# Performance work log

Hardware: AMD Instinct MI355X
Metric: run time of the kernel (lower is better)

Reference implementation:

```python
import jax, jax.numpy as jnp
import numpy as np

RMIN, RMAX, MAX_PHASE = 0.9, 1.0, 6.283


def setup_inputs() -> dict:
    key = jax.random.key(0)
    ks = jax.random.split(key, 12)
    Bsz, T, U, O, S, H = 16, 4096, 128, 128, 256, 512
    inp = jax.random.normal(ks[0], (Bsz, T, U), dtype=jnp.float32)
    # stable complex diagonal: |lambda| in [RMIN, RMAX], phase in [0, MAX_PHASE]
    r = RMIN + (RMAX - RMIN) * jax.random.uniform(ks[1], (S,), dtype=jnp.float32)
    theta = MAX_PHASE * jax.random.uniform(ks[2], (S,), dtype=jnp.float32)
    Lambda_re = r * jnp.cos(theta)
    Lambda_im = r * jnp.sin(theta)
    B = jax.random.normal(ks[3], (S, U), dtype=jnp.float32) / np.sqrt(U)
    C = jax.random.normal(ks[4], (O, S), dtype=jnp.float32) / np.sqrt(S)
    D = jax.random.normal(ks[5], (O, U), dtype=jnp.float32) / np.sqrt(U)
    W1 = jax.random.normal(ks[6], (H, O), dtype=jnp.float32) / np.sqrt(O)
    W2 = jax.random.normal(ks[7], (H, H), dtype=jnp.float32) / np.sqrt(H)
    W3 = jax.random.normal(ks[8], (O, H), dtype=jnp.float32) / np.sqrt(H)
    Wlin = jax.random.normal(ks[9], (O, U), dtype=jnp.float32) / np.sqrt(U)
    return {"input": inp, "Lambda_re": Lambda_re, "Lambda_im": Lambda_im,
            "B": B, "C": C, "D": D, "W1": W1, "W2": W2, "W3": W3, "Wlin": Wlin}


def _linear_scan(lam, bu):
    # lam: (S,) complex; bu: (B, T, S) complex
    # h_t = lam * h_{t-1} + bu_t, h_0 = 0  (work-efficient associative scan)
    A = jnp.broadcast_to(lam[None, None, :], bu.shape)

    def combine(c1, c2):
        a1, x1 = c1
        a2, x2 = c2
        return a1 * a2, a2 * x1 + x2

    _, h = jax.lax.associative_scan(combine, (A, bu), axis=1)
    return h


def reference(input, Lambda_re, Lambda_im, B, C, D, W1, W2, W3, Wlin):
    lam = (Lambda_re + 1j * Lambda_im).astype(jnp.complex64)        # (S,)
    bu = jnp.einsum('btu,su->bts', input, B).astype(jnp.complex64)   # (B,T,S)
    h = _linear_scan(lam, bu)                                        # (B,T,S) complex
    # LRU readout: real(C h) + D u
    y = jnp.einsum('bts,os->bto', h, C.astype(jnp.complex64)).real \
        + jnp.einsum('btu,ou->bto', input, D)                        # (B,T,O)
    # MLP: Linear->SiLU->Linear->ReLU->Linear (no biases)
    z = jax.nn.silu(y @ W1.T)
    z = jax.nn.relu(z @ W2.T)
    mlp_out = z @ W3.T                                               # (B,T,O)
    # residual linear path
    return mlp_out + input @ Wlin.T
```

## Files before the change

### kernel.cpp

```cpp
#include <hip/hip_runtime.h>
#include <hip/hip_bf16.h>

#define BSZ 16
#define TT 4096
#define UU 128
#define OO 128
#define SS 256
#define HH 512
#define BT (BSZ*TT)
#define CLEN 64
#define NCH (TT/CLEN)

using bf16x8 = __attribute__((ext_vector_type(8))) short;
using f32x4  = __attribute__((ext_vector_type(4))) float;

__device__ __forceinline__ unsigned short f2bf(float x){
  union { float f; unsigned int u; } v; v.f = x;
  unsigned int r = v.u + 0x7fffu + ((v.u >> 16) & 1u);
  return (unsigned short)(r >> 16);
}
__device__ __forceinline__ float bf2f(unsigned short h){
  union { float f; unsigned int u; } v; v.u = ((unsigned int)h) << 16;
  return v.f;
}

#define GLD16(g, s) __builtin_amdgcn_global_load_lds( \
    (const __attribute__((address_space(1))) unsigned int*)(g), \
    (__attribute__((address_space(3))) unsigned int*)(s), 16, 0, 0)

#define SBAR() do{ __builtin_amdgcn_sched_barrier(0); \
                   __builtin_amdgcn_s_barrier(); \
                   __builtin_amdgcn_sched_barrier(0); }while(0)

__global__ __launch_bounds__(256) void split_k(const float* __restrict__ x,
                                               unsigned short* __restrict__ H,
                                               unsigned short* __restrict__ L, int n4){
  int i = blockIdx.x * 256 + threadIdx.x;
  if (i >= n4) return;
  float4 v = ((const float4*)x)[i];
  unsigned short h0 = f2bf(v.x), h1 = f2bf(v.y), h2 = f2bf(v.z), h3 = f2bf(v.w);
  ushort4 hh = make_ushort4(h0, h1, h2, h3);
  ushort4 ll = make_ushort4(f2bf(v.x - bf2f(h0)), f2bf(v.y - bf2f(h1)),
                            f2bf(v.z - bf2f(h2)), f2bf(v.w - bf2f(h3)));
  ((ushort4*)H)[i] = hh;
  ((ushort4*)L)[i] = ll;
}

struct WJobs {
  const float* src[7];
  unsigned short* H[7];
  unsigned short* L[7];
  int end4[7];
};
__global__ __launch_bounds__(256) void split_w(WJobs j, int total4){
  int i = blockIdx.x * 256 + threadIdx.x;
  if (i >= total4) return;
  int t = 0, base = 0;
  #pragma unroll
  for (int k = 0; k < 7; k++){
    if (i >= j.end4[k]){ t = k + 1; base = j.end4[k]; }
  }
  int idx = i - base;
  float4 v = ((const float4*)j.src[t])[idx];
  unsigned short h0 = f2bf(v.x), h1 = f2bf(v.y), h2 = f2bf(v.z), h3 = f2bf(v.w);
  ushort4 hh = make_ushort4(h0, h1, h2, h3);
  ushort4 ll = make_ushort4(f2bf(v.x - bf2f(h0)), f2bf(v.y - bf2f(h1)),
                            f2bf(v.z - bf2f(h2)), f2bf(v.w - bf2f(h3)));
  ((ushort4*)j.H[t])[idx] = hh;
  ((ushort4*)j.L[t])[idx] = ll;
}

__global__ __launch_bounds__(256, 2) void gemm_split(
    const unsigned short* __restrict__ AH1, const unsigned short* __restrict__ AL1,
    const unsigned short* __restrict__ BH1, const unsigned short* __restrict__ BL1, int K1, int f1,
    const unsigned short* __restrict__ AH2, const unsigned short* __restrict__ AL2,
    const unsigned short* __restrict__ BH2, const unsigned short* __restrict__ BL2, int K2, int f2,
    unsigned short* __restrict__ outH, unsigned short* __restrict__ outL,
    float* __restrict__ outF, int Nout, int EPI,
    const float* __restrict__ lre, const float* __restrict__ lim,
    float2* __restrict__ ends)
{
  __shared__ __align__(16) unsigned short SM[32768];
  unsigned short* Ah = SM;
  unsigned short* Al = SM + 8192;
  unsigned short* Bh = SM + 16384;
  unsigned short* Bl = SM + 24576;

  const int tid = threadIdx.x;
  const int mb = blockIdx.x, nb = blockIdx.y;
  const int l = tid & 63, w = tid >> 6;
  const int wr = w >> 1, wc = w & 1;
  const int fr = l & 15, fq = l >> 4;

  f32x4 acc[4][4];
  #pragma unroll
  for (int m = 0; m < 4; m++)
    #pragma unroll
    for (int n = 0; n < 4; n++) acc[m][n] = f32x4{0.f, 0.f, 0.f, 0.f};

  const int nkt = (K1 + K2) >> 5;

  auto STAGE = [&](int buf, int kt){
    const int k0 = kt << 5;
    const unsigned short *aH, *aL, *bH, *bL; int st, kk, flg;
    if (k0 < K1){ aH = AH1; aL = AL1; bH = BH1; bL = BL1; st = K1; kk = k0; flg = f1; }
    else        { aH = AH2; aL = AL2; bH = BH2; bL = BL2; st = K2; kk = k0 - K1; flg = f2; }
    #pragma unroll
    for (int it = 0; it < 2; it++){
      int seg = tid + it * 256;
      int r = seg >> 2, c4 = seg & 3;
      int sc = (c4 ^ ((r >> 1) & 3)) << 3;
      size_t go = (size_t)(mb*128 + r) * st + kk + sc;
      size_t gb = (size_t)(nb*128 + r) * st + kk + sc;
      int lo = buf*4096 + r*32 + c4*8;
      GLD16(aH + go, Ah + lo);
      if (flg & 1) GLD16(aL + go, Al + lo);
      GLD16(bH + gb, Bh + lo);
      if (flg & 2) GLD16(bL + gb, Bl + lo);
    }
  };

  STAGE(0, 0);
  __syncthreads();

  for (int kt = 0; kt < nkt; kt++){
    const int cur = kt & 1;
    const int flg = ((kt << 5) < K1) ? f1 : f2;
    if (kt + 1 < nkt) STAGE(cur ^ 1, kt + 1);

    bf16x8 a_h[4], a_l[4], b_h[4], b_l[4];
    #pragma unroll
    for (int m = 0; m < 4; m++){
      int lra = wr*64 + m*16 + fr;
      int ra = cur*4096 + lra*32 + ((fq ^ ((lra >> 1) & 3)) << 3);
      a_h[m] = *(const bf16x8*)&Ah[ra];
      if (flg & 1) a_l[m] = *(const bf16x8*)&Al[ra];
      int lrb = wc*64 + m*16 + fr;
      int rb = cur*4096 + lrb*32 + ((fq ^ ((lrb >> 1) & 3)) << 3);
      b_h[m] = *(const bf16x8*)&Bh[rb];
      if (flg & 2) b_l[m] = *(const bf16x8*)&Bl[rb];
    }
    __builtin_amdgcn_s_setprio(1);
    #pragma unroll
    for (int m = 0; m < 4; m++)
      #pragma unroll
      for (int n = 0; n < 4; n++)
        acc[m][n] = __builtin_amdgcn_mfma_f32_16x16x32_bf16(a_h[m], b_h[n], acc[m][n], 0, 0, 0);
    if (flg & 1)
      #pragma unroll
      for (int m = 0; m < 4; m++)
        #pragma unroll
        for (int n = 0; n < 4; n++)
          acc[m][n] = __builtin_amdgcn_mfma_f32_16x16x32_bf16(a_l[m], b_h[n], acc[m][n], 0, 0, 0);
    if (flg & 2)
      #pragma unroll
      for (int m = 0; m < 4; m++)
        #pragma unroll
        for (int n = 0; n < 4; n++)
          acc[m][n] = __builtin_amdgcn_mfma_f32_16x16x32_bf16(a_h[m], b_l[n], acc[m][n], 0, 0, 0);
    __builtin_amdgcn_s_setprio(0);

    __syncthreads();
  }

  float* fl = (float*)SM;
  #pragma unroll
  for (int m = 0; m < 4; m++)
    #pragma unroll
    for (int n = 0; n < 4; n++)
      #pragma unroll
      for (int j = 0; j < 4; j++)
        fl[(wr*64 + m*16 + fq*4 + j)*128 + wc*64 + n*16 + fr] = acc[m][n][j];
  __syncthreads();
  #pragma unroll
  for (int it = 0; it < 8; it++){
    int task = tid + (it << 8);
    int rl = task >> 4, cg = task & 15;
    float4 v0 = *(const float4*)&fl[rl*128 + cg*8];
    float4 v1 = *(const float4*)&fl[rl*128 + cg*8 + 4];
    size_t o = (size_t)(mb*128 + rl) * Nout + nb*128 + cg*8;
    if (EPI == 0){
      *(float4*)(outF + o)     = v0;
      *(float4*)(outF + o + 4) = v1;
    } else {
      float xv[8] = {v0.x,v0.y,v0.z,v0.w,v1.x,v1.y,v1.z,v1.w};
      union { unsigned short us[8]; uint4 v; } ph, pl;
      #pragma unroll
      for (int e = 0; e < 8; e++){
        float x = xv[e];
        if (EPI == 2)      x = x / (1.f + __expf(-x));
        else if (EPI == 3) x = fmaxf(x, 0.f);
        ph.us[e] = f2bf(x);
        pl.us[e] = f2bf(x - bf2f(ph.us[e]));
      }
      *(uint4*)(outH + o) = ph.v;
      if (outL) *(uint4*)(outL + o) = pl.v;
    }
  }
  if (ends){
    int c = tid >> 7, sl = tid & 127;
    int b = mb >> 5, chunk = ((mb & 31) << 1) + c;
    int s = nb*128 + sl;
    float lr = lre[s], li = lim[s];
    float hr = 0.f, hi2 = 0.f;
    for (int t = 0; t < 64; t++){
      float x = fl[(c*64 + t)*128 + sl];
      float nr = fmaf(lr, hr, fmaf(-li, hi2, x));
      float ni = fmaf(lr, hi2, li * hr);
      hr = nr; hi2 = ni;
    }
    ends[((size_t)(b*NCH + chunk))*SS + s] = make_float2(hr, hi2);
  }
}

#define WS_OFF 65536
#define YOFF   131072

__global__ __launch_bounds__(512, 1) void mlp_fused(
    const unsigned short* __restrict__ yH,
    const unsigned short* __restrict__ W1H,
    const unsigned short* __restrict__ W2H,
    unsigned short* __restrict__ z2H)
{
  __shared__ __align__(16) unsigned char LDS[163840];
  const int tid = threadIdx.x;
  const int l = tid & 63, w = tid >> 6;
  const int fr = l & 15, fq = l >> 4;
  const size_t r0 = (size_t)blockIdx.x * 64;

  const unsigned short* w2base[4];
  int w2lds[4];
  #pragma unroll
  for (int it = 0; it < 4; it++){
    int seg = l + (it << 6);
    int r = seg >> 2, c4 = seg & 3;
    w2base[it] = W2H + (size_t)(w*64 + r) * HH + ((c4 ^ ((r >> 1) & 3)) << 3);
    w2lds[it] = WS_OFF + w*12288 + seg*16;
  }
  auto stageW2 = [&](int kt){
    const int so = (kt % 3) * 4096;
    #pragma unroll
    for (int it = 0; it < 4; it++)
      GLD16(w2base[it] + kt*32, LDS + w2lds[it] + so);
  };

  #pragma unroll
  for (int it = 0; it < 16; it++){
    int seg = tid + (it << 9);
    int r = seg >> 4, c16 = seg & 15;
    GLD16(W1H + (size_t)r * UU + ((c16 ^ (r & 7)) << 3), LDS + seg*16);
  }
  #pragma unroll
  for (int it = 0; it < 2; it++){
    int seg = tid + (it << 9);
    int r = seg >> 4, c16 = seg & 15;
    GLD16(yH + (size_t)(r0 + r) * UU + ((c16 ^ (r & 7)) << 3),
          LDS + YOFF + seg*16);
  }
  asm volatile("s_waitcnt vmcnt(0)" ::: "memory");
  SBAR();

  f32x4 acc[4][4];
  #pragma unroll
  for (int m = 0; m < 4; m++)
    #pragma unroll
    for (int n = 0; n < 4; n++) acc[m][n] = f32x4{0.f, 0.f, 0.f, 0.f};

  #pragma unroll
  for (int kt = 0; kt < 4; kt++){
    bf16x8 a[4], b[4];
    #pragma unroll
    for (int m = 0; m < 4; m++){
      int row = m*16 + fr, kc = kt*4 + fq;
      a[m] = *(const bf16x8*)(LDS + YOFF + (row*128 + ((kc ^ (row & 7)) << 3))*2);
    }
    #pragma unroll
    for (int n = 0; n < 4; n++){
      int lrb = w*64 + n*16 + fr, kc = kt*4 + fq;
      b[n] = *(const bf16x8*)(LDS + (lrb*128 + ((kc ^ (lrb & 7)) << 3))*2);
    }
    __builtin_amdgcn_s_setprio(1);
    #pragma unroll
    for (int m = 0; m < 4; m++)
      #pragma unroll
      for (int n = 0; n < 4; n++)
        acc[m][n] = __builtin_amdgcn_mfma_f32_16x16x32_bf16(a[m], b[n], acc[m][n], 0, 0, 0);
    __builtin_amdgcn_s_setprio(0);
  }
  SBAR();

  stageW2(0);
  stageW2(1);

  unsigned short* Z1 = (unsigned short*)LDS;
  #pragma unroll
  for (int m = 0; m < 4; m++)
    #pragma unroll
    for (int n = 0; n < 4; n++)
      #pragma unroll
      for (int j = 0; j < 4; j++){
        float x = acc[m][n][j];
        x = x / (1.f + __expf(-x));
        int row = m*16 + fq*4 + j;
        int col = w*64 + n*16 + fr;
        Z1[(col >> 3)*512 + row*8 + (col & 7)] = f2bf(x);
      }
  SBAR();

  #pragma unroll
  for (int m = 0; m < 4; m++)
    #pragma unroll
    for (int n = 0; n < 4; n++) acc[m][n] = f32x4{0.f, 0.f, 0.f, 0.f};

  for (int kt = 0; kt < 16; kt++){
    if (kt < 15) asm volatile("s_waitcnt vmcnt(4)" ::: "memory");
    else         asm volatile("s_waitcnt vmcnt(0)" ::: "memory");
    __builtin_amdgcn_sched_barrier(0);
    const unsigned char* Wb = LDS + WS_OFF + w*12288 + (kt % 3)*4096;
    bf16x8 a[4], b[4];
    #pragma unroll
    for (int m = 0; m < 4; m++)
      a[m] = *(const bf16x8*)(LDS + (size_t)(kt*4 + fq)*1024 + (m*16 + fr)*16);
    #pragma unroll
    for (int n = 0; n < 4; n++){
      int rl = n*16 + fr;
      b[n] = *(const bf16x8*)(Wb + rl*64 + ((fq ^ ((rl >> 1) & 3)) << 4));
    }
    __builtin_amdgcn_s_setprio(1);
    #pragma unroll
    for (int m = 0; m < 4; m++)
      #pragma unroll
      for (int n = 0; n < 4; n++)
        acc[m][n] = __builtin_amdgcn_mfma_f32_16x16x32_bf16(a[m], b[n], acc[m][n], 0, 0, 0);
    __builtin_amdgcn_s_setprio(0);
    if (kt + 2 < 16) stageW2(kt + 2);
  }
  SBAR();

  unsigned short* EP = (unsigned short*)(LDS + WS_OFF);
  #pragma unroll
  for (int m = 0; m < 4; m++)
    #pragma unroll
    for (int n = 0; n < 4; n++)
      #pragma unroll
      for (int j = 0; j < 4; j++){
        float x = fmaxf(acc[m][n][j], 0.f);
        EP[(m*16 + fq*4 + j)*512 + w*64 + n*16 + fr] = f2bf(x);
      }
  __syncthreads();
  #pragma unroll
  for (int it = 0; it < 8; it++){
    int seg = tid + (it << 9);
    int r = seg >> 6, c8 = seg & 63;
    *(uint4*)(z2H + (r0 + r)*HH + c8*8) = *(const uint4*)&EP[r*512 + c8*8];
  }
}

__global__ __launch_bounds__(256) void scan_carries(const float2* __restrict__ ends,
                                                    const float* __restrict__ lre,
                                                    const float* __restrict__ lim,
                                                    float2* __restrict__ carryin){
  const int idx = blockIdx.x * 256 + threadIdx.x;
  const int b = idx >> 8;
  const int s = idx & 255;
  float pr = lre[s], pi = lim[s];
  #pragma unroll
  for (int q = 0; q < 6; q++){
    float nr = pr*pr - pi*pi;
    float ni = 2.f * pr * pi;
    pr = nr; pi = ni;
  }
  float hr = 0.f, hi = 0.f;
  for (int c = 0; c < NCH; c++){
    size_t o = ((size_t)b*NCH + c)*SS + s;
    carryin[o] = make_float2(hr, hi);
    float2 e = ends[o];
    float nr = fmaf(pr, hr, fmaf(-pi, hi, e.x));
    float ni = fmaf(pr, hi, fmaf(pi, hr, e.y));
    hr = nr; hi = ni;
  }
}

__global__ __launch_bounds__(256) void scan_apply_v(
    const unsigned short* __restrict__ buH, const unsigned short* __restrict__ buL,
    const float* __restrict__ lre, const float* __restrict__ lim,
    const float2* __restrict__ carryin, unsigned short* __restrict__ RehH){
  const int tid = threadIdx.x;
  const int grp = tid >> 6, ln = tid & 63;
  const int chunk = blockIdx.x * 4 + grp;
  const int b = chunk >> 6, ch = chunk & 63;
  const int s0 = ln * 4;
  float lr[4], li[4], hr[4], hi[4];
  #pragma unroll
  for (int e = 0; e < 4; e++){ lr[e] = lre[s0+e]; li[e] = lim[s0+e]; }
  const float2* ci = &carryin[((size_t)(b*NCH + ch))*SS + s0];
  #pragma unroll
  for (int e = 0; e < 4; e++){ hr[e] = ci[e].x; hi[e] = ci[e].y; }
  const size_t rbase = ((size_t)b*TT + (size_t)ch*CLEN)*SS + s0;
  for (int t = 0; t < CLEN; t++){
    uint2 hv = *(const uint2*)(buH + rbase + (size_t)t*SS);
    uint2 lv = *(const uint2*)(buL + rbase + (size_t)t*SS);
    const unsigned short* hs = (const unsigned short*)&hv;
    const unsigned short* ls = (const unsigned short*)&lv;
    uint2 ov; unsigned short* os = (unsigned short*)&ov;
    #pragma unroll
    for (int e = 0; e < 4; e++){
      float x = bf2f(hs[e]) + bf2f(ls[e]);
      float nr = fmaf(lr[e], hr[e], fmaf(-li[e], hi[e], x));
      float ni = fmaf(lr[e], hi[e], li[e] * hr[e]);
      hr[e] = nr; hi[e] = ni;
      os[e] = f2bf(nr);
    }
    *(uint2*)(RehH + rbase + (size_t)t*SS) = ov;
  }
}

extern "C" void kernel_launch(void* const* d_in, const int* in_sizes, int n_in,
                              void* d_out, int out_size, void* d_ws, size_t ws_size,
                              hipStream_t stream){
  const float* inp = (const float*)d_in[0];
  const float* lre = (const float*)d_in[1];
  const float* lim = (const float*)d_in[2];
  const float* Bm  = (const float*)d_in[3];
  const float* Cm  = (const float*)d_in[4];
  const float* Dm  = (const float*)d_in[5];
  const float* W1  = (const float*)d_in[6];
  const float* W2  = (const float*)d_in[7];
  const float* W3  = (const float*)d_in[8];
  const float* Wl  = (const float*)d_in[9];
  float* out = (float*)d_out;

  char* ws = (char*)d_ws;
  size_t off = 0;
  auto alloc = [&](size_t bytes)->char*{
    char* p = ws + off; off += (bytes + 255) & ~(size_t)255; return p;
  };
  unsigned short* inH  = (unsigned short*)alloc((size_t)BT*UU*2);
  unsigned short* inL  = (unsigned short*)alloc((size_t)BT*UU*2);
  char* Rbu = alloc((size_t)BT*SS*2*2);
  unsigned short* buH = (unsigned short*)Rbu;
  unsigned short* buL = (unsigned short*)(Rbu + (size_t)BT*SS*2);
  char* R2 = alloc((size_t)BT*HH*2);
  unsigned short* RehH = (unsigned short*)R2;
  unsigned short* yH   = (unsigned short*)(R2 + (size_t)BT*SS*2);
  unsigned short* z2H  = (unsigned short*)Rbu;
  unsigned short* BwH = (unsigned short*)alloc((size_t)SS*UU*2);
  unsigned short* BwL = (unsigned short*)alloc((size_t)SS*UU*2);
  unsigned short* CH_ = (unsigned short*)alloc((size_t)OO*SS*2);
  unsigned short* CL_ = (unsigned short*)alloc((size_t)OO*SS*2);
  unsigned short* DH_ = (unsigned short*)alloc((size_t)OO*UU*2);
  unsigned short* DL_ = (unsigned short*)alloc((size_t)OO*UU*2);
  unsigned short* W1H = (unsigned short*)alloc((size_t)HH*OO*2);
  unsigned short* W1L = (unsigned short*)alloc((size_t)HH*OO*2);
  unsigned short* W2H = (unsigned short*)alloc((size_t)HH*HH*2);
  unsigned short* W2L = (unsigned short*)alloc((size_t)HH*HH*2);
  unsigned short* W3H = (unsigned short*)alloc((size_t)OO*HH*2);
  unsigned short* W3L = (unsigned short*)alloc((size_t)OO*HH*2);
  unsigned short* WlH = (unsigned short*)alloc((size_t)OO*UU*2);
  unsigned short* WlL = (unsigned short*)alloc((size_t)OO*UU*2);
  float2* ends    = (float2*)alloc((size_t)BSZ*NCH*SS*8);
  float2* carryin = (float2*)alloc((size_t)BSZ*NCH*SS*8);
  if (off > ws_size) return;

  split_k<<<(BT*UU/4 + 255)/256, 256, 0, stream>>>(inp, inH, inL, BT*UU/4);
  {
    WJobs j;
    const float* srcs[7] = {Bm, Cm, Dm, W1, W2, W3, Wl};
    unsigned short* Hs[7] = {BwH, CH_, DH_, W1H, W2H, W3H, WlH};
    unsigned short* Ls[7] = {BwL, CL_, DL_, W1L, W2L, W3L, WlL};
    int n4s[7] = {SS*UU/4, OO*SS/4, OO*UU/4, HH*OO/4, HH*HH/4, OO*HH/4, OO*UU/4};
    int cum = 0;
    for (int k = 0; k < 7; k++){
      j.src[k] = srcs[k]; j.H[k] = Hs[k]; j.L[k] = Ls[k];
      cum += n4s[k]; j.end4[k] = cum;
    }
    split_w<<<(cum + 255)/256, 256, 0, stream>>>(j, cum);
  }

  gemm_split<<<dim3(BT/128, SS/128), 256, 0, stream>>>(
      inH, inL, BwH, BwL, UU, 3,
      inH, inL, BwH, BwL, 0,  3,
      buH, buL, nullptr, SS, 1,
      lre, lim, ends);

  scan_carries<<<(BSZ*SS)/256, 256, 0, stream>>>(ends, lre, lim, carryin);

  scan_apply_v<<<BSZ*NCH/4, 256, 0, stream>>>(buH, buL, lre, lim, carryin, RehH);

  gemm_split<<<dim3(BT/128, OO/128), 256, 0, stream>>>(
      RehH, RehH, CH_, CL_, SS, 2,
      inH,  inL,  DH_, DL_, UU, 3,
      yH, nullptr, nullptr, OO, 1,
      nullptr, nullptr, nullptr);

  mlp_fused<<<BT/64, 512, 0, stream>>>(yH, W1H, W2H, z2H);

  gemm_split<<<dim3(BT/128, OO/128), 256, 0, stream>>>(
      z2H, z2H, W3H, W3L, HH, 2,
      inH, inL, WlH, WlL, UU, 3,
      nullptr, nullptr, out, OO, 0,
      nullptr, nullptr, nullptr);
}
```

Measured before the change: 207.6 us.

## Split fused MLP across 16 waves and stream W1 through the LDS ring

The fused MLP kernel now runs with 1024 threads instead of 512. Each of the 16 waves computes 32 output columns instead of 64, which halves per-wave accumulators and B fragments. W1 is no longer loaded whole into LDS up front. It is streamed in k-slices through the same triple-buffered per-wave ring as W2, so the first GEMM overlaps global loads with MFMA work and LDS use shrinks. The cost is that every wave re-reads the shared A (y / Z1) fragments, so LDS read traffic for A roughly doubles, and the block uses more barriers.

Result: no change. 204.8 us (-1.4%).

```diff
diff --git a/kernel.cpp b/kernel.cpp
--- a/kernel.cpp
+++ b/kernel.cpp
@@ -213,10 +213,9 @@
   }
 }
 
-#define WS_OFF 65536
-#define YOFF   131072
-
-__global__ __launch_bounds__(512, 1) void mlp_fused(
+#define RING_OFF 65536
+
+__global__ __launch_bounds__(1024, 1) void mlp_fused(
     const unsigned short* __restrict__ yH,
     const unsigned short* __restrict__ W1H,
     const unsigned short* __restrict__ W2H,
@@ -228,64 +227,68 @@
   const int fr = l & 15, fq = l >> 4;
   const size_t r0 = (size_t)blockIdx.x * 64;
 
-  const unsigned short* w2base[4];
-  int w2lds[4];
-  #pragma unroll
-  for (int it = 0; it < 4; it++){
+  const unsigned short* w1base[2];
+  const unsigned short* w2base[2];
+  int rlds[2];
+  #pragma unroll
+  for (int it = 0; it < 2; it++){
     int seg = l + (it << 6);
     int r = seg >> 2, c4 = seg & 3;
-    w2base[it] = W2H + (size_t)(w*64 + r) * HH + ((c4 ^ ((r >> 1) & 3)) << 3);
-    w2lds[it] = WS_OFF + w*12288 + seg*16;
-  }
+    int sc = (c4 ^ ((r >> 1) & 3)) << 3;
+    w1base[it] = W1H + (size_t)(w*32 + r) * UU + sc;
+    w2base[it] = W2H + (size_t)(w*32 + r) * HH + sc;
+    rlds[it] = RING_OFF + w*6144 + seg*16;
+  }
+  auto stageW1 = [&](int kt){
+    const int so = (kt % 3) * 2048;
+    #pragma unroll
+    for (int it = 0; it < 2; it++) GLD16(w1base[it] + kt*32, LDS + rlds[it] + so);
+  };
   auto stageW2 = [&](int kt){
-    const int so = (kt % 3) * 4096;
-    #pragma unroll
-    for (int it = 0; it < 4; it++)
-      GLD16(w2base[it] + kt*32, LDS + w2lds[it] + so);
+    const int so = (kt % 3) * 2048;
+    #pragma unroll
+    for (int it = 0; it < 2; it++) GLD16(w2base[it] + kt*32, LDS + rlds[it] + so);
   };
 
-  #pragma unroll
-  for (int it = 0; it < 16; it++){
-    int seg = tid + (it << 9);
-    int r = seg >> 4, c16 = seg & 15;
-    GLD16(W1H + (size_t)r * UU + ((c16 ^ (r & 7)) << 3), LDS + seg*16);
-  }
-  #pragma unroll
-  for (int it = 0; it < 2; it++){
-    int seg = tid + (it << 9);
-    int r = seg >> 4, c16 = seg & 15;
-    GLD16(yH + (size_t)(r0 + r) * UU + ((c16 ^ (r & 7)) << 3),
-          LDS + YOFF + seg*16);
-  }
-  asm volatile("s_waitcnt vmcnt(0)" ::: "memory");
+  {
+    int r = tid >> 4, c16 = tid & 15;
+    GLD16(yH + (size_t)(r0 + r) * UU + ((c16 ^ (r & 7)) << 3), LDS + tid*16);
+  }
+  stageW1(0);
+  stageW1(1);
+  asm volatile("s_waitcnt vmcnt(4)" ::: "memory");
   SBAR();
 
-  f32x4 acc[4][4];
+  f32x4 acc[4][2];
   #pragma unroll
   for (int m = 0; m < 4; m++)
     #pragma unroll
-    for (int n = 0; n < 4; n++) acc[m][n] = f32x4{0.f, 0.f, 0.f, 0.f};
-
-  #pragma unroll
+    for (int n = 0; n < 2; n++) acc[m][n] = f32x4{0.f, 0.f, 0.f, 0.f};
+
   for (int kt = 0; kt < 4; kt++){
-    bf16x8 a[4], b[4];
+    if (kt < 3) asm volatile("s_waitcnt vmcnt(2)" ::: "memory");
+    else        asm volatile("s_waitcnt vmcnt(0)" ::: "memory");
+    __builtin_amdgcn_sched_barrier(0);
+    const unsigned char* Wb = LDS + RING_OFF + w*6144 + (kt % 3)*2048;
+    bf16x8 a[4], b[2];
     #pragma unroll
     for (int m = 0; m < 4; m++){
       int row = m*16 + fr, kc = kt*4 + fq;
-      a[m] = *(const bf16x8*)(LDS + YOFF + (row*128 + ((kc ^ (row & 7)) << 3))*2);
-    }
-    #pragma unroll
-    for (int n = 0; n < 4; n++){
-      int lrb = w*64 + n*16 + fr, kc = kt*4 + fq;
-      b[n] = *(const bf16x8*)(LDS + (lrb*128 + ((kc ^ (lrb & 7)) << 3))*2);
+      a[m] = *(const bf16x8*)(LDS + (row*128 + ((kc ^ (row & 7)) << 3))*2);
+    }
+    #pragma unroll
+    for (int n = 0; n < 2; n++){
+      int rl = n*16 + fr;
+      b[n] = *(const bf16x8*)(Wb + rl*64 + ((fq ^ ((rl >> 1) & 3)) << 4));
     }
     __builtin_amdgcn_s_setprio(1);
     #pragma unroll
     for (int m = 0; m < 4; m++)
       #pragma unroll
-      for (int n = 0; n < 4; n++)
+      for (int n = 0; n < 2; n++)
         acc[m][n] = __builtin_amdgcn_mfma_f32_16x16x32_bf16(a[m], b[n], acc[m][n], 0, 0, 0);
     __builtin_amdgcn_s_setprio(0);
+    if (kt + 2 < 4) stageW1(kt + 2);
   }
   SBAR();
 
@@ -296,13 +299,13 @@
   #pragma unroll
   for (int m = 0; m < 4; m++)
     #pragma unroll
-    for (int n = 0; n < 4; n++)
+    for (int n = 0; n < 2; n++)
       #pragma unroll
       for (int j = 0; j < 4; j++){
         float x = acc[m][n][j];
         x = x / (1.f + __expf(-x));
         int row = m*16 + fq*4 + j;
-        int col = w*64 + n*16 + fr;
+        int col = w*32 + n*16 + fr;
         Z1[(col >> 3)*512 + row*8 + (col & 7)] = f2bf(x);
       }
   SBAR();
@@ -310,19 +313,19 @@
   #pragma unroll
   for (int m = 0; m < 4; m++)
     #pragma unroll
-    for (int n = 0; n < 4; n++) acc[m][n] = f32x4{0.f, 0.f, 0.f, 0.f};
+    for (int n = 0; n < 2; n++) acc[m][n] = f32x4{0.f, 0.f, 0.f, 0.f};
 
   for (int kt = 0; kt < 16; kt++){
-    if (kt < 15) asm volatile("s_waitcnt vmcnt(4)" ::: "memory");
+    if (kt < 15) asm volatile("s_waitcnt vmcnt(2)" ::: "memory");
     else         asm volatile("s_waitcnt vmcnt(0)" ::: "memory");
     __builtin_amdgcn_sched_barrier(0);
-    const unsigned char* Wb = LDS + WS_OFF + w*12288 + (kt % 3)*4096;
-    bf16x8 a[4], b[4];
+    const unsigned char* Wb = LDS + RING_OFF + w*6144 + (kt % 3)*2048;
+    bf16x8 a[4], b[2];
     #pragma unroll
     for (int m = 0; m < 4; m++)
       a[m] = *(const bf16x8*)(LDS + (size_t)(kt*4 + fq)*1024 + (m*16 + fr)*16);
     #pragma unroll
-    for (int n = 0; n < 4; n++){
+    for (int n = 0; n < 2; n++){
       int rl = n*16 + fr;
       b[n] = *(const bf16x8*)(Wb + rl*64 + ((fq ^ ((rl >> 1) & 3)) << 4));
     }
@@ -330,27 +333,27 @@
     #pragma unroll
     for (int m = 0; m < 4; m++)
       #pragma unroll
-      for (int n = 0; n < 4; n++)
+      for (int n = 0; n < 2; n++)
         acc[m][n] = __builtin_amdgcn_mfma_f32_16x16x32_bf16(a[m], b[n], acc[m][n], 0, 0, 0);
     __builtin_amdgcn_s_setprio(0);
     if (kt + 2 < 16) stageW2(kt + 2);
   }
   SBAR();
 
-  unsigned short* EP = (unsigned short*)(LDS + WS_OFF);
+  unsigned short* EP = (unsigned short*)(LDS + RING_OFF);
   #pragma unroll
   for (int m = 0; m < 4; m++)
     #pragma unroll
-    for (int n = 0; n < 4; n++)
+    for (int n = 0; n < 2; n++)
       #pragma unroll
       for (int j = 0; j < 4; j++){
         float x = fmaxf(acc[m][n][j], 0.f);
-        EP[(m*16 + fq*4 + j)*512 + w*64 + n*16 + fr] = f2bf(x);
+        EP[(m*16 + fq*4 + j)*512 + w*32 + n*16 + fr] = f2bf(x);
       }
   __syncthreads();
   #pragma unroll
-  for (int it = 0; it < 8; it++){
-    int seg = tid + (it << 9);
+  for (int it = 0; it < 4; it++){
+    int seg = tid + (it << 10);
     int r = seg >> 6, c8 = seg & 63;
     *(uint4*)(z2H + (r0 + r)*HH + c8*8) = *(const uint4*)&EP[r*512 + c8*8];
   }
@@ -493,7 +496,7 @@
       yH, nullptr, nullptr, OO, 1,
       nullptr, nullptr, nullptr);
 
-  mlp_fused<<<BT/64, 512, 0, stream>>>(yH, W1H, W2H, z2H);
+  mlp_fused<<<BT/64, 1024, 0, stream>>>(yH, W1H, W2H, z2H);
 
   gemm_split<<<dim3(BT/128, OO/128), 256, 0, stream>>>(
       z2H, z2H, W3H, W3L, HH, 2,
```
